# Kernel optimization log

Hardware: AMD Instinct MI355X
Metric: run time of the kernel (lower is better)

The kernel has to match this reference:

```python
import jax, jax.numpy as jnp
import numpy as np

B, H, P, K, E, BN = 8, 256, 1024, 32, 4, 64


def setup_inputs() -> dict:
    key = jax.random.key(0)
    ks = jax.random.split(key, 8)
    current = jax.random.normal(ks[0], (B, H, P), dtype=jnp.float32)
    neighbor_features = jax.random.normal(ks[1], (B, H, P, K), dtype=jnp.float32)
    # binary {0,1} validity mask, stored as float like the torch module expects
    neighbor_validity = jax.random.randint(ks[2], (B, 1, P, K), 0, 2).astype(jnp.float32)
    edge_features = jax.random.normal(ks[3], (B, E, P, K), dtype=jnp.float32)
    # 1x1 Conv2d weights flattened to matrices: (out_ch, in_ch)
    w1 = jax.random.normal(ks[4], (BN, 2 * H + E), dtype=jnp.float32) * 0.05
    b1 = jnp.zeros((BN,), dtype=jnp.float32)
    w2 = jax.random.normal(ks[5], (BN,), dtype=jnp.float32) * 0.05  # second conv: out_ch=1
    b2 = jnp.zeros((), dtype=jnp.float32)
    return {
        "current": current,
        "neighbor_features": neighbor_features,
        "neighbor_validity": neighbor_validity,
        "edge_features": edge_features,
        "w1": w1,
        "b1": b1,
        "w2": w2,
        "b2": b2,
    }


def reference(current, neighbor_features, neighbor_validity, edge_features, w1, b1, w2, b2):
    h_dim = current.shape[1]
    # Split the 1x1-conv weight along the concat axis so we never materialize
    # the [B, 2H+E, P, K] concatenated tensor (same math as cat + conv1x1).
    w1c = w1[:, :h_dim]            # acts on broadcast center features
    w1n = w1[:, h_dim:2 * h_dim]   # acts on neighbor features
    w1e = w1[:, 2 * h_dim:]        # acts on edge features

    hid = (
        jnp.einsum("bcp,oc->bop", current, w1c)[:, :, :, None]
        + jnp.einsum("bcpk,oc->bopk", neighbor_features, w1n)
        + jnp.einsum("bcpk,oc->bopk", edge_features, w1e)
        + b1[None, :, None, None]
    )
    hid = jax.nn.relu(hid)                                  # (B, BN, P, K)
    logits = jnp.einsum("bopk,o->bpk", hid, w2) + b2        # (B, P, K)

    valid = neighbor_validity[:, 0] > 0.5                   # (B, P, K) bool
    logits = jnp.where(valid, logits, -jnp.inf)
    has_any = jnp.any(valid, axis=-1, keepdims=True)        # (B, P, 1)
    logits_safe = jnp.where(has_any, logits, 0.0)           # all-masked rows -> 0 logits
    weights = jax.nn.softmax(logits_safe, axis=-1)
    weights = jnp.where(has_any & valid, weights, 0.0)      # zero weight on pads / empty rows

    pooled = jnp.einsum("bcpk,bpk->bcp", neighbor_features, weights)
    return pooled
```

## Files before the change

### kernel.cpp

```cpp
#include <hip/hip_runtime.h>
#include <math.h>


#define B_ 8
#define H_ 256
#define P_ 1024
#define K_ 32
#define E_ 4
#define BN_ 64

typedef __attribute__((ext_vector_type(8))) short short8;
typedef __attribute__((ext_vector_type(4))) float floatx4;

__device__ __forceinline__ unsigned short bf16_rne(float f) {
  unsigned u = __float_as_uint(f);
  u += 0x7fffu + ((u >> 16) & 1u);
  return (unsigned short)(u >> 16);
}
__device__ __forceinline__ unsigned pack_bf16(float lo, float hi) {
  unsigned r;
  asm("v_cvt_pk_bf16_f32 %0, %1, %2" : "=v"(r) : "v"(lo), "v"(hi));
  return r;
}

__device__ __forceinline__ void async_cp16(const float* g, float* l) {
  __builtin_amdgcn_global_load_lds(
      (const __attribute__((address_space(1))) unsigned*)g,
      (__attribute__((address_space(3))) unsigned*)l, 16, 0, 0);
}

__device__ __forceinline__ unsigned* tile_ptr(unsigned* tile, int n, int cp) {
  return tile + n * 128 + ((((cp >> 2) ^ (n & 7)) << 2) | (cp & 3));
}

#define STR_(x) #x
#define VMWAIT(n) asm volatile("s_waitcnt vmcnt(" STR_(n) ")")

__global__ __launch_bounds__(256) void prep_kernel(
    const float* __restrict__ w1, unsigned short* __restrict__ w1m) {
  int i = blockIdx.x * 256 + threadIdx.x;
  if (i >= 4 * 17 * 64 * 8) return;
  int j = i & 7, lane = (i >> 3) & 63;
  int kt = i >> 9;
  int mt = kt / 17, ki = kt % 17;
  int o = mt * 16 + (lane & 15);
  int c = ki * 32 + (lane >> 4) * 8 + j;
  float v = (c < 516) ? w1[o * 516 + c] : 0.f;
  w1m[i] = bf16_rne(v);
}

__global__ __launch_bounds__(256, 2) void soft_attn_agg_kernel(
    const float* __restrict__ cur,
    const float* __restrict__ nf,
    const float* __restrict__ nv,
    const float* __restrict__ ef,
    const unsigned short* __restrict__ w1m,
    const float* __restrict__ b1,
    const float* __restrict__ w2,
    float* __restrict__ out) {
  __shared__ unsigned s_tile[128 * 128];
  __shared__ float s_raw[3 * 8 * 128];
  __shared__ unsigned short s_curb[4][264];
  __shared__ unsigned s_edge[4][32][2];
  __shared__ float s_b1v[BN_];
  __shared__ float s_w2v[BN_];
  float* const s_lg = s_raw;
  float* const s_wt = s_raw + 128;

  const int t = threadIdx.x;
  const unsigned bid = blockIdx.x;
  const unsigned xcd = bid & 7u, sx = bid >> 3;
  const int b = (int)(sx >> 5);
  const int pg = (int)(xcd * 32u + (sx & 31u));
  const int p0 = pg * 4;

  const int w = t >> 6;
  const int lane = t & 63;
  const int q = lane >> 4;
  const int ln15 = lane & 15;

  const float* nf_b = nf + ((size_t)b * H_ * P_ + p0) * K_;

#define ISSUE_DMA(ch, bufbase)                                               \
  async_cp16(nf_b + (size_t)((ch)*8 + 2 * w + (lane >> 5)) * (P_ * K_) +     \
                 ((lane & 31) << 2),                                         \
             (bufbase) + 2 * w * 128)

  float* const rbuf0 = s_raw;
  float* const rbuf1 = s_raw + 1024;
  float* const rbuf2 = s_raw + 2048;

  ISSUE_DMA(0, rbuf0);
  ISSUE_DMA(1, rbuf1);
  ISSUE_DMA(2, rbuf2);

  {
    const float* cb = cur + ((size_t)b * H_ + t) * P_ + p0;
    float4 ca = *(const float4*)cb;
    s_curb[0][t] = bf16_rne(ca.x);
    s_curb[1][t] = bf16_rne(ca.y);
    s_curb[2][t] = bf16_rne(ca.z);
    s_curb[3][t] = bf16_rne(ca.w);
  }
  float my_valid = 0.f;
  if (t < 128) {
    my_valid = nv[((size_t)b * P_ + p0) * K_ + t];
    const int pl = t >> 5, k = t & 31;
    const float* ep = ef + ((size_t)b * E_ * P_ + p0 + pl) * K_ + k;
    float e0 = ep[0];
    float e1 = ep[(size_t)(P_ * K_)];
    float e2 = ep[(size_t)(2 * P_ * K_)];
    float e3 = ep[(size_t)(3 * P_ * K_)];
    s_edge[pl][k][0] = pack_bf16(e0, e1);
    s_edge[pl][k][1] = pack_bf16(e2, e3);
  } else if (t < 192) {
    s_b1v[t - 128] = b1[t - 128];
  } else {
    s_w2v[t - 192] = w2[t - 192];
  }

#define PIPE_ITER(ch, bufbase, VMN, DO_ISSUE)                                \
  {                                                                          \
    VMWAIT(VMN);                                                             \
    __builtin_amdgcn_sched_barrier(0);                                       \
    const float* rb0 = (bufbase) + 2 * w * 128;                              \
    const float* rb1 = rb0 + 128;                                            \
    float fe0 = rb0[lane], fo0 = rb1[lane];                                  \
    float fe1 = rb0[lane + 64], fo1 = rb1[lane + 64];                        \
    unsigned pk0 = pack_bf16(fe0, fo0);                                      \
    unsigned pk1 = pack_bf16(fe1, fo1);                                      \
    __builtin_amdgcn_sched_barrier(0);                                       \
    if (DO_ISSUE) ISSUE_DMA((ch) + 3, bufbase);                              \
    const int cpv = 4 * (ch) + w;                                            \
    *tile_ptr(s_tile, lane, cpv) = pk0;                                      \
    *tile_ptr(s_tile, lane + 64, cpv) = pk1;                                 \
  }

  for (int c3 = 0; c3 < 30; c3 += 3) {
    PIPE_ITER(c3, rbuf0, 2, (c3) < 29);
    PIPE_ITER(c3 + 1, rbuf1, 2, (c3 + 1) < 29);
    PIPE_ITER(c3 + 2, rbuf2, 2, (c3 + 2) < 29);
  }
  PIPE_ITER(30, rbuf0, 1, false);
  PIPE_ITER(31, rbuf1, 0, false);
  __syncthreads();

  floatx4 acc[4][2];
#pragma unroll
  for (int mt = 0; mt < 4; ++mt) {
    floatx4 binit = *(const floatx4*)&s_b1v[mt * 16 + q * 4];
    acc[mt][0] = binit;
    acc[mt][1] = binit;
  }
  const unsigned short* w1m_l = w1m + (size_t)lane * 8;

#pragma unroll
  for (int ki = 0; ki < 8; ++ki) {
    short8 bc = *(const short8*)&s_curb[w][ki * 32 + q * 8];
#pragma unroll
    for (int mt = 0; mt < 4; ++mt) {
      short8 a = *(const short8*)(w1m_l + (size_t)(mt * 17 + ki) * 512);
      acc[mt][0] = __builtin_amdgcn_mfma_f32_16x16x32_bf16(a, bc, acc[mt][0], 0, 0, 0);
      acc[mt][1] = __builtin_amdgcn_mfma_f32_16x16x32_bf16(a, bc, acc[mt][1], 0, 0, 0);
    }
  }
#pragma unroll
  for (int ck = 0; ck < 8; ++ck) {
    short8 bn0 = *(const short8*)tile_ptr(s_tile, 32 * w + ln15, (4 * ck + q) << 2);
    short8 bn1 = *(const short8*)tile_ptr(s_tile, 32 * w + 16 + ln15, (4 * ck + q) << 2);
#pragma unroll
    for (int mt = 0; mt < 4; ++mt) {
      short8 a = *(const short8*)(w1m_l + (size_t)(mt * 17 + 8 + ck) * 512);
      acc[mt][0] = __builtin_amdgcn_mfma_f32_16x16x32_bf16(a, bn0, acc[mt][0], 0, 0, 0);
      acc[mt][1] = __builtin_amdgcn_mfma_f32_16x16x32_bf16(a, bn1, acc[mt][1], 0, 0, 0);
    }
  }
  {
    union { unsigned u[4]; short8 s; } ub0, ub1;
    *(uint2*)&ub0.u[0] = *(const uint2*)&s_edge[w][ln15][0];
    ub0.u[2] = 0u; ub0.u[3] = 0u;
    *(uint2*)&ub1.u[0] = *(const uint2*)&s_edge[w][16 + ln15][0];
    ub1.u[2] = 0u; ub1.u[3] = 0u;
#pragma unroll
    for (int mt = 0; mt < 4; ++mt) {
      short8 a = *(const short8*)(w1m_l + (size_t)(mt * 17 + 16) * 512);
      acc[mt][0] = __builtin_amdgcn_mfma_f32_16x16x32_bf16(a, ub0.s, acc[mt][0], 0, 0, 0);
      acc[mt][1] = __builtin_amdgcn_mfma_f32_16x16x32_bf16(a, ub1.s, acc[mt][1], 0, 0, 0);
    }
  }

#pragma unroll
  for (int nti = 0; nti < 2; ++nti) {
    float lp = 0.f;
#pragma unroll
    for (int mt = 0; mt < 4; ++mt) {
      const floatx4 w2v = *(const floatx4*)&s_w2v[mt * 16 + q * 4];
#pragma unroll
      for (int r = 0; r < 4; ++r)
        lp = fmaf(fmaxf(acc[mt][nti][r], 0.f), w2v[r], lp);
    }
    lp += __shfl_xor(lp, 16);
    lp += __shfl_xor(lp, 32);
    if (lane < 16) s_lg[(2 * w + nti) * 16 + ln15] = lp;
  }
  __syncthreads();

  if (t < 128) {
    float lg = s_lg[t];
    bool v = my_valid > 0.5f;
    float ml = v ? lg : -INFINITY;
#pragma unroll
    for (int m = 1; m < 32; m <<= 1) ml = fmaxf(ml, __shfl_xor(ml, m));
    float e = v ? __expf(lg - ml) : 0.f;
    float ssum = e;
#pragma unroll
    for (int m = 1; m < 32; m <<= 1) ssum += __shfl_xor(ssum, m);
    s_wt[t] = (ml > -INFINITY) ? (e / ssum) : 0.f;
  }
  __syncthreads();

  {
    const int cpr = t & 127, ph = t >> 7;
    const int nb = ph * 64;
    float a0e = 0.f, a0o = 0.f, a1e = 0.f, a1o = 0.f;
#pragma unroll
    for (int k = 0; k < K_; ++k) {
      const unsigned u0 = *tile_ptr(s_tile, nb + k, cpr);
      const unsigned u1 = *tile_ptr(s_tile, nb + 32 + k, cpr);
      const float wt0 = s_wt[nb + k];
      const float wt1 = s_wt[nb + 32 + k];
      a0e = fmaf(__uint_as_float(u0 << 16), wt0, a0e);
      a0o = fmaf(__uint_as_float(u0 & 0xffff0000u), wt0, a0o);
      a1e = fmaf(__uint_as_float(u1 << 16), wt1, a1e);
      a1o = fmaf(__uint_as_float(u1 & 0xffff0000u), wt1, a1o);
    }
    float* op = out + ((size_t)b * H_ + 2 * cpr) * P_ + p0 + 2 * ph;
    float2 ve; ve.x = a0e; ve.y = a1e;
    float2 vo; vo.x = a0o; vo.y = a1o;
    *(float2*)op = ve;
    *(float2*)(op + P_) = vo;
  }
}

extern "C" void kernel_launch(void* const* d_in, const int* in_sizes, int n_in,
                              void* d_out, int out_size, void* d_ws,
                              size_t ws_size, hipStream_t stream) {
  const float* cur = (const float*)d_in[0];
  const float* nf  = (const float*)d_in[1];
  const float* nv  = (const float*)d_in[2];
  const float* ef  = (const float*)d_in[3];
  const float* w1  = (const float*)d_in[4];
  const float* b1  = (const float*)d_in[5];
  const float* w2  = (const float*)d_in[6];

  unsigned short* w1m = (unsigned short*)d_ws;
  prep_kernel<<<(4 * 17 * 64 * 8 + 255) / 256, 256, 0, stream>>>(w1, w1m);
  soft_attn_agg_kernel<<<B_ * P_ / 4, 256, 0, stream>>>(
      cur, nf, nv, ef, w1m, b1, w2, (float*)d_out);
}
```

Before: 399.6 us.

## Replace LDS DMA triple-buffer with register-prefetched global loads, eight chunks deep

Neighbor-feature chunks used to be staged with async global-to-LDS copies into a three-deep raw LDS ring. They are now loaded straight into registers with plain global loads, prefetched eight chunks ahead, then packed to bf16 and written into the swizzled tile. This drops the intermediate LDS round trip and the 12 KB raw buffer and allows more loads in flight. In exchange it uses many more VGPRs (128 floats of prefetch state), which may reduce occupancy or cause spills under the launch bound of 2 blocks.

```diff
diff --git a/kernel.cpp b/kernel.cpp
--- a/kernel.cpp
+++ b/kernel.cpp
@@ -23,18 +23,9 @@
   return r;
 }
 
-__device__ __forceinline__ void async_cp16(const float* g, float* l) {
-  __builtin_amdgcn_global_load_lds(
-      (const __attribute__((address_space(1))) unsigned*)g,
-      (__attribute__((address_space(3))) unsigned*)l, 16, 0, 0);
-}
-
 __device__ __forceinline__ unsigned* tile_ptr(unsigned* tile, int n, int cp) {
   return tile + n * 128 + ((((cp >> 2) ^ (n & 7)) << 2) | (cp & 3));
 }
-
-#define STR_(x) #x
-#define VMWAIT(n) asm volatile("s_waitcnt vmcnt(" STR_(n) ")")
 
 __global__ __launch_bounds__(256) void prep_kernel(
     const float* __restrict__ w1, unsigned short* __restrict__ w1m) {
@@ -59,13 +50,12 @@
     const float* __restrict__ w2,
     float* __restrict__ out) {
   __shared__ unsigned s_tile[128 * 128];
-  __shared__ float s_raw[3 * 8 * 128];
   __shared__ unsigned short s_curb[4][264];
   __shared__ unsigned s_edge[4][32][2];
   __shared__ float s_b1v[BN_];
   __shared__ float s_w2v[BN_];
-  float* const s_lg = s_raw;
-  float* const s_wt = s_raw + 128;
+  __shared__ float s_lg[128];
+  __shared__ float s_wt[128];
 
   const int t = threadIdx.x;
   const unsigned bid = blockIdx.x;
@@ -79,70 +69,70 @@
   const int q = lane >> 4;
   const int ln15 = lane & 15;
 
+  const int PKr = P_ * K_;
   const float* nf_b = nf + ((size_t)b * H_ * P_ + p0) * K_;
 
-#define ISSUE_DMA(ch, bufbase)                                               \
-  async_cp16(nf_b + (size_t)((ch)*8 + 2 * w + (lane >> 5)) * (P_ * K_) +     \
-                 ((lane & 31) << 2),                                         \
-             (bufbase) + 2 * w * 128)
-
-  float* const rbuf0 = s_raw;
-  float* const rbuf1 = s_raw + 1024;
-  float* const rbuf2 = s_raw + 2048;
-
-  ISSUE_DMA(0, rbuf0);
-  ISSUE_DMA(1, rbuf1);
-  ISSUE_DMA(2, rbuf2);
-
-  {
-    const float* cb = cur + ((size_t)b * H_ + t) * P_ + p0;
-    float4 ca = *(const float4*)cb;
-    s_curb[0][t] = bf16_rne(ca.x);
-    s_curb[1][t] = bf16_rne(ca.y);
-    s_curb[2][t] = bf16_rne(ca.z);
-    s_curb[3][t] = bf16_rne(ca.w);
-  }
-  float my_valid = 0.f;
+  float4 ca = *(const float4*)(cur + ((size_t)b * H_ + t) * P_ + p0);
+  float sv = 0.f, e0 = 0.f, e1 = 0.f, e2 = 0.f, e3 = 0.f, bw = 0.f;
   if (t < 128) {
-    my_valid = nv[((size_t)b * P_ + p0) * K_ + t];
+    sv = nv[((size_t)b * P_ + p0) * K_ + t];
     const int pl = t >> 5, k = t & 31;
     const float* ep = ef + ((size_t)b * E_ * P_ + p0 + pl) * K_ + k;
-    float e0 = ep[0];
-    float e1 = ep[(size_t)(P_ * K_)];
-    float e2 = ep[(size_t)(2 * P_ * K_)];
-    float e3 = ep[(size_t)(3 * P_ * K_)];
+    e0 = ep[0];
+    e1 = ep[(size_t)PKr];
+    e2 = ep[(size_t)(2 * PKr)];
+    e3 = ep[(size_t)(3 * PKr)];
+  } else if (t < 192) {
+    bw = b1[t - 128];
+  } else {
+    bw = w2[t - 192];
+  }
+
+  float ve0[32], ve1[32], vo0[32], vo1[32];
+#define ISSUE_CH(ch)                                       \
+  {                                                        \
+    const float* re = nf_b + (size_t)(8 * (ch) + 2 * w) * PKr; \
+    const float* ro = re + PKr;                            \
+    ve0[ch] = re[lane];                                    \
+    ve1[ch] = re[lane + 64];                               \
+    vo0[ch] = ro[lane];                                    \
+    vo1[ch] = ro[lane + 64];                               \
+  }
+#define CONSUME_CH(ch)                                     \
+  {                                                        \
+    unsigned pk0 = pack_bf16(ve0[ch], vo0[ch]);            \
+    unsigned pk1 = pack_bf16(ve1[ch], vo1[ch]);            \
+    const int cpv = 4 * (ch) + w;                          \
+    *tile_ptr(s_tile, lane, cpv) = pk0;                    \
+    *tile_ptr(s_tile, lane + 64, cpv) = pk1;               \
+  }
+
+#pragma unroll
+  for (int ch = 0; ch < 8; ++ch) ISSUE_CH(ch);
+  __builtin_amdgcn_sched_barrier(0);
+
+  s_curb[0][t] = bf16_rne(ca.x);
+  s_curb[1][t] = bf16_rne(ca.y);
+  s_curb[2][t] = bf16_rne(ca.z);
+  s_curb[3][t] = bf16_rne(ca.w);
+  float my_valid = sv;
+  if (t < 128) {
+    const int pl = t >> 5, k = t & 31;
     s_edge[pl][k][0] = pack_bf16(e0, e1);
     s_edge[pl][k][1] = pack_bf16(e2, e3);
   } else if (t < 192) {
-    s_b1v[t - 128] = b1[t - 128];
+    s_b1v[t - 128] = bw;
   } else {
-    s_w2v[t - 192] = w2[t - 192];
-  }
-
-#define PIPE_ITER(ch, bufbase, VMN, DO_ISSUE)                                \
-  {                                                                          \
-    VMWAIT(VMN);                                                             \
-    __builtin_amdgcn_sched_barrier(0);                                       \
-    const float* rb0 = (bufbase) + 2 * w * 128;                              \
-    const float* rb1 = rb0 + 128;                                            \
-    float fe0 = rb0[lane], fo0 = rb1[lane];                                  \
-    float fe1 = rb0[lane + 64], fo1 = rb1[lane + 64];                        \
-    unsigned pk0 = pack_bf16(fe0, fo0);                                      \
-    unsigned pk1 = pack_bf16(fe1, fo1);                                      \
-    __builtin_amdgcn_sched_barrier(0);                                       \
-    if (DO_ISSUE) ISSUE_DMA((ch) + 3, bufbase);                              \
-    const int cpv = 4 * (ch) + w;                                            \
-    *tile_ptr(s_tile, lane, cpv) = pk0;                                      \
-    *tile_ptr(s_tile, lane + 64, cpv) = pk1;                                 \
-  }
-
-  for (int c3 = 0; c3 < 30; c3 += 3) {
-    PIPE_ITER(c3, rbuf0, 2, (c3) < 29);
-    PIPE_ITER(c3 + 1, rbuf1, 2, (c3 + 1) < 29);
-    PIPE_ITER(c3 + 2, rbuf2, 2, (c3 + 2) < 29);
-  }
-  PIPE_ITER(30, rbuf0, 1, false);
-  PIPE_ITER(31, rbuf1, 0, false);
+    s_w2v[t - 192] = bw;
+  }
+  __builtin_amdgcn_sched_barrier(0);
+
+#pragma unroll
+  for (int ch = 0; ch < 32; ++ch) {
+    if (ch < 24) ISSUE_CH(ch + 8);
+    CONSUME_CH(ch);
+    __builtin_amdgcn_sched_barrier(0);
+  }
   __syncthreads();
 
   floatx4 acc[4][2];
```

After: 397.0 us. No clear change (-0.7%).
